# Kernel tuning notes

Measured on AMD Instinct MI355X. Metric: run time of the kernel, lower is better.

## Reference

```python
import jax, jax.numpy as jnp
import numpy as np

OUT_FEATURES = 8192
IN_FEATURES = 8192
BATCH = 512


def setup_inputs() -> dict:
    key = jax.random.key(0)
    k_x, k_w, k_s = jax.random.split(key, 3)
    x = jax.random.normal(k_x, (BATCH, IN_FEATURES), dtype=jnp.float32)
    # packed int4 weights: each int holds two nibbles (values 0..255)
    packed_weight = jax.random.randint(k_w, (OUT_FEATURES, IN_FEATURES // 2), 0, 256, dtype=jnp.int32)
    # per-output-row scale (positive, as produced by abs-max quantization)
    scale = jax.random.uniform(k_s, (OUT_FEATURES, 1), dtype=jnp.float32) * 0.02 + 1e-4
    return {"x": x, "packed_weight": packed_weight, "scale": scale}


def reference(x, packed_weight, scale):
    # Unpack two 4-bit values per byte: high nibble first (matches torch loop:
    # col i <- packed >> 4 & 15, col i+1 <- packed & 15), then subtract zero-point 8.
    hi = (packed_weight >> 4) & 15
    lo = packed_weight & 15
    q = jnp.stack([hi, lo], axis=-1).reshape(OUT_FEATURES, IN_FEATURES) - 8  # [out, in] int
    w = q.astype(scale.dtype) * scale  # dequantized weight [out, in]
    # linear: y = x @ W^T
    return jnp.einsum('bi,oi->bo', x, w)
```

## Files before the change

### kernel.cpp

```cpp
#include <hip/hip_runtime.h>
#include <cstdint>
#include <cstddef>

#define IN_F 8192
#define OUT_F 8192
#define BATCH 512
#define KSPLIT 2
#define KSLICE (IN_F / KSPLIT)
#define BK 64
#define TILES (KSLICE / BK)
#define BM 128
#define BN 256

typedef __bf16 bf16x8 __attribute__((ext_vector_type(8)));
typedef float floatx4 __attribute__((ext_vector_type(4)));

__device__ __forceinline__ ushort f2bf(float f) {
  uint32_t u = __float_as_uint(f);
  u += 0x7FFFu + ((u >> 16) & 1u);
  return (ushort)(u >> 16);
}

__device__ __forceinline__ uint32_t dq(int p) {
  uint32_t u = (uint32_t)p;
  return (((u >> 4) & 0xFu) | ((u & 0xFu) << 16)) | 0x43004300u;
}

__device__ __forceinline__ void gl16(const void* g, uint32_t* l) {
  __builtin_amdgcn_global_load_lds(
      (const __attribute__((address_space(1))) uint32_t*)g,
      (__attribute__((address_space(3))) uint32_t*)l, 16, 0, 0);
}

__global__ __launch_bounds__(256) void cvt_rowsum(const float* __restrict__ x,
                                                  ushort* __restrict__ xb,
                                                  float* __restrict__ rowsum,
                                                  float* __restrict__ zout) {
  const int b = blockIdx.x;
  const int t = threadIdx.x;
  const float4* xr = (const float4*)(x + (size_t)b * IN_F);
  ushort4* xo = (ushort4*)(xb + (size_t)b * IN_F);
  float s[2] = {0.f, 0.f};
#pragma unroll
  for (int i = 0; i < 8; ++i) {
    float4 v = xr[i * 256 + t];
    ushort4 o;
    o.x = f2bf(v.x); o.y = f2bf(v.y); o.z = f2bf(v.z); o.w = f2bf(v.w);
    xo[i * 256 + t] = o;
    if (zout) {
      float4 z = {0.f, 0.f, 0.f, 0.f};
      ((float4*)(zout + (size_t)b * OUT_F))[i * 256 + t] = z;
    }
    s[i >> 2] += __uint_as_float((uint32_t)o.x << 16) + __uint_as_float((uint32_t)o.y << 16)
               + __uint_as_float((uint32_t)o.z << 16) + __uint_as_float((uint32_t)o.w << 16);
  }
  __shared__ float red[4][2];
  const int lane = t & 63, wid = t >> 6;
#pragma unroll
  for (int j = 0; j < 2; ++j) {
    float v = s[j];
#pragma unroll
    for (int off = 32; off >= 1; off >>= 1) v += __shfl_down(v, off, 64);
    if (lane == 0) red[wid][j] = v;
  }
  __syncthreads();
  if (t < 2) rowsum[t * BATCH + b] = red[0][t] + red[1][t] + red[2][t] + red[3][t];
}

__global__ __launch_bounds__(512, 2) void qgemm(const ushort* __restrict__ xb,
                                                const int* __restrict__ pw,
                                                const float* __restrict__ scale,
                                                const float* __restrict__ rowsum,
                                                float* __restrict__ out,
                                                float* __restrict__ part) {
  __shared__ uint32_t As[2 * BM * 32];
  __shared__ uint32_t Bs[2 * BN * 32];

  const int tid = threadIdx.x;
  const int lane = tid & 63;
  const int w = tid >> 6;
  const int wm = w >> 2, wn = w & 3;
  const int lr = lane & 15, lq = lane >> 4;

  const int n0 = blockIdx.x * BN;
  const int m0 = blockIdx.y * BM;
  const int ks = blockIdx.z;

  const char* aSrc = (const char*)xb
      + (size_t)(m0 + w * 16 + (lane >> 3)) * (IN_F * 2)
      + (size_t)ks * (KSLICE * 2)
      + (size_t)((((lane & 7) ^ ((lane >> 3) & 7)) * 16));
  uint32_t* aDst = As + (w * 16) * 32;

  const int rt = tid >> 1;
  const int c0 = (tid & 1) * 2;
  const int rk = rt & 7;
  const int* bSrc = pw + (size_t)(n0 + rt) * (IN_F / 2) + ks * (KSLICE / 2);

  const int key = lr & 7;
  const int aOff = (wm * 64 + lr) * 32 + ((lq ^ key) * 4);
  const int bOff = (wn * 64 + lr) * 32 + ((lq ^ key) * 4);

  floatx4 acc[4][4] = {};

  auto stB = [&](int nb, int q, int4 p) {
    int4 u;
    u.x = dq(p.x); u.y = dq(p.y); u.z = dq(p.z); u.w = dq(p.w);
    *(int4*)(Bs + nb * 8192 + rt * 32 + ((q ^ rk) * 4)) = u;
  };

#define RD_BV(kh)                                                            \
  _Pragma("unroll") for (int fn = 0; fn < 4; ++fn)                           \
      bv[fn] = *(const bf16x8*)(Bs + (((bOff + fn * 512) ^ ((kh)*16)) + buf * 8192));
#define RD_AV(kh)                                                            \
  _Pragma("unroll") for (int fm = 0; fm < 4; ++fm)                           \
      av[fm] = *(const bf16x8*)(As + (((aOff + fm * 512) ^ ((kh)*16)) + buf * 4096));
#define MFMA_BLK()                                                           \
  __builtin_amdgcn_s_setprio(1);                                             \
  _Pragma("unroll") for (int fm = 0; fm < 4; ++fm)                           \
      _Pragma("unroll") for (int fn = 0; fn < 4; ++fn)                       \
          acc[fm][fn] = __builtin_amdgcn_mfma_f32_16x16x32_bf16(             \
              av[fm], bv[fn], acc[fm][fn], 0, 0, 0);                         \
  __builtin_amdgcn_s_setprio(0);

  {
    int4 p0 = *(const int4*)(bSrc + c0 * 4);
    int4 p1 = *(const int4*)(bSrc + c0 * 4 + 4);
    int4 p2 = *(const int4*)(bSrc + (c0 + 4) * 4);
    int4 p3 = *(const int4*)(bSrc + (c0 + 4) * 4 + 4);
    stB(0, c0, p0); stB(0, c0 + 1, p1); stB(0, c0 + 4, p2); stB(0, c0 + 5, p3);
    gl16(aSrc, aDst);
    gl16(aSrc + 131072, aDst + 256);
    asm volatile("s_waitcnt lgkmcnt(0)" ::: "memory");
  }

  for (int t = 0; t < TILES - 1; ++t) {
    const int buf = t & 1, nb = buf ^ 1;
    const int* bs = bSrc + (t + 1) * 32;
    int4 pb0 = *(const int4*)(bs + c0 * 4);
    int4 pb1 = *(const int4*)(bs + c0 * 4 + 4);
    int4 pb2 = *(const int4*)(bs + (c0 + 4) * 4);
    int4 pb3 = *(const int4*)(bs + (c0 + 4) * 4 + 4);
    const char* as = aSrc + (size_t)(t + 1) * 128;
    gl16(as, aDst + nb * 4096);
    gl16(as + 131072, aDst + nb * 4096 + 256);
    asm volatile("s_waitcnt vmcnt(6)" ::: "memory");
    asm volatile("s_barrier" ::: "memory");

    bf16x8 av[4], bv[4];
    RD_BV(0); RD_AV(0);
    MFMA_BLK();
    RD_BV(1); RD_AV(1);
    MFMA_BLK();
    stB(nb, c0, pb0); stB(nb, c0 + 1, pb1);
    stB(nb, c0 + 4, pb2); stB(nb, c0 + 5, pb3);

    asm volatile("s_waitcnt lgkmcnt(0)" ::: "memory");
    asm volatile("s_barrier" ::: "memory");
  }

  {
    const int buf = (TILES - 1) & 1;
    asm volatile("s_waitcnt vmcnt(0)" ::: "memory");
    asm volatile("s_barrier" ::: "memory");
    bf16x8 av[4], bv[4];
    RD_BV(0); RD_AV(0);
    MFMA_BLK();
    RD_BV(1); RD_AV(1);
    MFMA_BLK();
  }

  const int omb = m0 + wm * 64 + lq * 4;
  const int on = n0 + wn * 64 + lr;
  float scv[4];
#pragma unroll
  for (int fn = 0; fn < 4; ++fn) scv[fn] = scale[on + fn * 16];
  float rsv[4][4];
#pragma unroll
  for (int mi = 0; mi < 4; ++mi)
#pragma unroll
    for (int rr = 0; rr < 4; ++rr)
      rsv[mi][rr] = rowsum[ks * BATCH + omb + mi * 16 + rr];

  if (part) {
    float* dst = ks ? part : out;
#pragma unroll
    for (int mi = 0; mi < 4; ++mi)
#pragma unroll
      for (int fn = 0; fn < 4; ++fn) {
        const float s = scv[fn];
        float* op = dst + (size_t)(omb + mi * 16) * OUT_F + (on + fn * 16);
#pragma unroll
        for (int rr = 0; rr < 4; ++rr)
          op[(size_t)rr * OUT_F] = s * (acc[mi][fn][rr] - 136.f * rsv[mi][rr]);
      }
  } else {
#pragma unroll
    for (int mi = 0; mi < 4; ++mi)
#pragma unroll
      for (int fn = 0; fn < 4; ++fn) {
        const float s = scv[fn];
        float* op = out + (size_t)(omb + mi * 16) * OUT_F + (on + fn * 16);
#pragma unroll
        for (int rr = 0; rr < 4; ++rr)
          atomicAdd(op + (size_t)rr * OUT_F, s * (acc[mi][fn][rr] - 136.f * rsv[mi][rr]));
      }
  }
#undef RD_BV
#undef RD_AV
#undef MFMA_BLK
}

__global__ __launch_bounds__(256) void reduce_add(float* __restrict__ out,
                                                  const float* __restrict__ part) {
  const size_t n = (size_t)BATCH * OUT_F / 4;
  float4* o4 = (float4*)out;
  const float4* p4 = (const float4*)part;
  for (size_t i = (size_t)blockIdx.x * 256 + threadIdx.x; i < n;
       i += (size_t)gridDim.x * 256) {
    float4 a = o4[i];
    float4 b = p4[i];
    a.x += b.x; a.y += b.y; a.z += b.z; a.w += b.w;
    o4[i] = a;
  }
}

extern "C" void kernel_launch(void* const* d_in, const int* in_sizes, int n_in,
                              void* d_out, int out_size, void* d_ws, size_t ws_size,
                              hipStream_t stream) {
  const float* x = (const float*)d_in[0];
  const int* pw = (const int*)d_in[1];
  const float* scale = (const float*)d_in[2];
  float* out = (float*)d_out;

  ushort* xb = (ushort*)d_ws;
  float* rowsum = (float*)((char*)d_ws + (size_t)8 * 1024 * 1024);
  const size_t need = (size_t)8 * 1024 * 1024 + 65536 + (size_t)BATCH * OUT_F * 4;
  float* part = (ws_size >= need)
      ? (float*)((char*)d_ws + (size_t)8 * 1024 * 1024 + 65536)
      : nullptr;

  cvt_rowsum<<<BATCH, 256, 0, stream>>>(x, xb, rowsum, part ? nullptr : out);
  dim3 grid(OUT_F / BN, BATCH / BM, KSPLIT);
  qgemm<<<grid, 512, 0, stream>>>(xb, pw, scale, rowsum, out, part);
  if (part) reduce_add<<<2048, 256, 0, stream>>>(out, part);
}
```

Measured before the change: 304.8 us.

## Deepen qgemm pipeline with 4-stage A buffer and register-prefetched B tiles

Restructures the qgemm main loop into a deeper software pipeline. The A tile now has four LDS buffers loaded two tiles ahead via global_load_lds, and packed B weights are prefetched two tiles ahead into registers and dequantised into LDS one tile ahead. Extra barriers split each k-step into two MFMA phases, with the next tile's stores interleaved between them, to hide global-load latency behind MFMA work. This raises LDS use (extra 32KB for A) and register pressure, which could hurt occupancy at 2 blocks per CU, and the added barriers add synchronisation cost.

After: 304.9 us. No clear change (+0.1%).

```diff
diff --git a/kernel.cpp b/kernel.cpp
--- a/kernel.cpp
+++ b/kernel.cpp
@@ -73,7 +73,7 @@
                                                 const float* __restrict__ rowsum,
                                                 float* __restrict__ out,
                                                 float* __restrict__ part) {
-  __shared__ uint32_t As[2 * BM * 32];
+  __shared__ uint32_t As[4 * BM * 32];
   __shared__ uint32_t Bs[2 * BN * 32];
 
   const int tid = threadIdx.x;
@@ -103,71 +103,102 @@
 
   floatx4 acc[4][4] = {};
 
-  auto stB = [&](int nb, int q, int4 p) {
+  auto stB = [&](int bow, int q, int4 p) {
     int4 u;
     u.x = dq(p.x); u.y = dq(p.y); u.z = dq(p.z); u.w = dq(p.w);
-    *(int4*)(Bs + nb * 8192 + rt * 32 + ((q ^ rk) * 4)) = u;
+    *(int4*)(Bs + bow + rt * 32 + ((q ^ rk) * 4)) = u;
   };
 
-#define RD_BV(kh)                                                            \
-  _Pragma("unroll") for (int fn = 0; fn < 4; ++fn)                           \
-      bv[fn] = *(const bf16x8*)(Bs + (((bOff + fn * 512) ^ ((kh)*16)) + buf * 8192));
-#define RD_AV(kh)                                                            \
-  _Pragma("unroll") for (int fm = 0; fm < 4; ++fm)                           \
-      av[fm] = *(const bf16x8*)(As + (((aOff + fm * 512) ^ ((kh)*16)) + buf * 4096));
-#define MFMA_BLK()                                                           \
+#define DSREAD(kh, AO, BO)                                                   \
+  _Pragma("unroll") for (int f = 0; f < 4; ++f)                              \
+      av[f] = *(const bf16x8*)(As + (((aOff + f * 512) ^ ((kh)*16)) + (AO))); \
+  _Pragma("unroll") for (int f = 0; f < 4; ++f)                              \
+      bv[f] = *(const bf16x8*)(Bs + (((bOff + f * 512) ^ ((kh)*16)) + (BO)));
+#define MFMA16()                                                             \
   __builtin_amdgcn_s_setprio(1);                                             \
   _Pragma("unroll") for (int fm = 0; fm < 4; ++fm)                           \
       _Pragma("unroll") for (int fn = 0; fn < 4; ++fn)                       \
           acc[fm][fn] = __builtin_amdgcn_mfma_f32_16x16x32_bf16(             \
               av[fm], bv[fn], acc[fm][fn], 0, 0, 0);                         \
   __builtin_amdgcn_s_setprio(0);
+#define BAR() asm volatile("s_barrier" ::: "memory")
+#define LGKM0()                                                              \
+  asm volatile("s_waitcnt lgkmcnt(0)" ::: "memory");                         \
+  __builtin_amdgcn_sched_barrier(0)
+
+  int4 pbC0, pbC1, pbC2, pbC3, pbN0, pbN1, pbN2, pbN3;
 
   {
-    int4 p0 = *(const int4*)(bSrc + c0 * 4);
-    int4 p1 = *(const int4*)(bSrc + c0 * 4 + 4);
-    int4 p2 = *(const int4*)(bSrc + (c0 + 4) * 4);
-    int4 p3 = *(const int4*)(bSrc + (c0 + 4) * 4 + 4);
-    stB(0, c0, p0); stB(0, c0 + 1, p1); stB(0, c0 + 4, p2); stB(0, c0 + 5, p3);
     gl16(aSrc, aDst);
     gl16(aSrc + 131072, aDst + 256);
-    asm volatile("s_waitcnt lgkmcnt(0)" ::: "memory");
-  }
-
-  for (int t = 0; t < TILES - 1; ++t) {
-    const int buf = t & 1, nb = buf ^ 1;
-    const int* bs = bSrc + (t + 1) * 32;
-    int4 pb0 = *(const int4*)(bs + c0 * 4);
-    int4 pb1 = *(const int4*)(bs + c0 * 4 + 4);
-    int4 pb2 = *(const int4*)(bs + (c0 + 4) * 4);
-    int4 pb3 = *(const int4*)(bs + (c0 + 4) * 4 + 4);
-    const char* as = aSrc + (size_t)(t + 1) * 128;
-    gl16(as, aDst + nb * 4096);
-    gl16(as + 131072, aDst + nb * 4096 + 256);
+    gl16(aSrc + 128, aDst + 4096);
+    gl16(aSrc + 128 + 131072, aDst + 4096 + 256);
+    int4 q0 = *(const int4*)(bSrc + c0 * 4);
+    int4 q1 = *(const int4*)(bSrc + c0 * 4 + 4);
+    int4 q2 = *(const int4*)(bSrc + (c0 + 4) * 4);
+    int4 q3 = *(const int4*)(bSrc + (c0 + 4) * 4 + 4);
+    stB(0, c0, q0); stB(0, c0 + 1, q1); stB(0, c0 + 4, q2); stB(0, c0 + 5, q3);
+    const int* b1 = bSrc + 32;
+    pbC0 = *(const int4*)(b1 + c0 * 4);
+    pbC1 = *(const int4*)(b1 + c0 * 4 + 4);
+    pbC2 = *(const int4*)(b1 + (c0 + 4) * 4);
+    pbC3 = *(const int4*)(b1 + (c0 + 4) * 4 + 4);
+    asm volatile("s_waitcnt vmcnt(0) lgkmcnt(0)" ::: "memory");
+    BAR();
+  }
+
+  for (int t = 0; t <= TILES - 3; ++t) {
+    const int AO = (t & 3) * 4096, BO = (t & 1) * 8192;
+    const int AOs = ((t + 2) & 3) * 4096, BOw = ((t + 1) & 1) * 8192;
+    bf16x8 av[4], bv[4];
+    const int* bs = bSrc + (t + 2) * 32;
+    pbN0 = *(const int4*)(bs + c0 * 4);
+    pbN1 = *(const int4*)(bs + c0 * 4 + 4);
+    pbN2 = *(const int4*)(bs + (c0 + 4) * 4);
+    pbN3 = *(const int4*)(bs + (c0 + 4) * 4 + 4);
+    DSREAD(0, AO, BO);
+    BAR(); LGKM0();
+    MFMA16();
+    BAR();
+    const char* as = aSrc + (size_t)(t + 2) * 128;
+    gl16(as, aDst + AOs);
+    gl16(as + 131072, aDst + AOs + 256);
+    stB(BOw, c0, pbC0); stB(BOw, c0 + 1, pbC1);
+    stB(BOw, c0 + 4, pbC2); stB(BOw, c0 + 5, pbC3);
+    DSREAD(1, AO, BO);
+    BAR(); LGKM0();
+    MFMA16();
     asm volatile("s_waitcnt vmcnt(6)" ::: "memory");
-    asm volatile("s_barrier" ::: "memory");
-
+    BAR();
+    pbC0 = pbN0; pbC1 = pbN1; pbC2 = pbN2; pbC3 = pbN3;
+  }
+
+  {
+    const int AO = ((TILES - 2) & 3) * 4096, BO = ((TILES - 2) & 1) * 8192;
+    const int BOw = ((TILES - 1) & 1) * 8192;
     bf16x8 av[4], bv[4];
-    RD_BV(0); RD_AV(0);
-    MFMA_BLK();
-    RD_BV(1); RD_AV(1);
-    MFMA_BLK();
-    stB(nb, c0, pb0); stB(nb, c0 + 1, pb1);
-    stB(nb, c0 + 4, pb2); stB(nb, c0 + 5, pb3);
-
-    asm volatile("s_waitcnt lgkmcnt(0)" ::: "memory");
-    asm volatile("s_barrier" ::: "memory");
-  }
-
+    DSREAD(0, AO, BO);
+    BAR(); LGKM0();
+    MFMA16();
+    BAR();
+    stB(BOw, c0, pbC0); stB(BOw, c0 + 1, pbC1);
+    stB(BOw, c0 + 4, pbC2); stB(BOw, c0 + 5, pbC3);
+    DSREAD(1, AO, BO);
+    BAR(); LGKM0();
+    MFMA16();
+    asm volatile("s_waitcnt vmcnt(0)" ::: "memory");
+    BAR();
+  }
   {
-    const int buf = (TILES - 1) & 1;
-    asm volatile("s_waitcnt vmcnt(0)" ::: "memory");
-    asm volatile("s_barrier" ::: "memory");
+    const int AO = ((TILES - 1) & 3) * 4096, BO = ((TILES - 1) & 1) * 8192;
     bf16x8 av[4], bv[4];
-    RD_BV(0); RD_AV(0);
-    MFMA_BLK();
-    RD_BV(1); RD_AV(1);
-    MFMA_BLK();
+    DSREAD(0, AO, BO);
+    BAR(); LGKM0();
+    MFMA16();
+    BAR();
+    DSREAD(1, AO, BO);
+    LGKM0();
+    MFMA16();
   }
 
   const int omb = m0 + wm * 64 + lq * 4;
@@ -206,9 +237,10 @@
           atomicAdd(op + (size_t)rr * OUT_F, s * (acc[mi][fn][rr] - 136.f * rsv[mi][rr]));
       }
   }
-#undef RD_BV
-#undef RD_AV
-#undef MFMA_BLK
+#undef DSREAD
+#undef MFMA16
+#undef BAR
+#undef LGKM0
 }
 
 __global__ __launch_bounds__(256) void reduce_add(float* __restrict__ out,
```

## Load packed weights directly into LDS with 4-stage async pipeline and dequant in registers

Applied to the files above, without the earlier changes.

The GEMM kernel is restructured to bring both activations and packed int4 weights into LDS with async global_load_lds through a 4-slot ring buffer. Weights are dequantized to bf16 in registers after the LDS read, using a cheaper nibble-extraction expression, instead of being dequantized before the LDS store. The tile grows to 256x256 with BK 32 and the K-split rises to 4, so rowsum and the reduction kernel are extended to handle three partial buffers. The aim is to hide global-load latency and remove the synchronous weight load-then-store stage, at the cost of more accumulator registers, a larger workspace and more partial-sum traffic.

Result: faster. 284.9 us (-6.5%).

```diff
diff --git a/kernel.cpp b/kernel.cpp
--- a/kernel.cpp
+++ b/kernel.cpp
@@ -5,11 +5,11 @@
 #define IN_F 8192
 #define OUT_F 8192
 #define BATCH 512
-#define KSPLIT 2
+#define KSPLIT 4
 #define KSLICE (IN_F / KSPLIT)
-#define BK 64
+#define BK 32
 #define TILES (KSLICE / BK)
-#define BM 128
+#define BM 256
 #define BN 256
 
 typedef __bf16 bf16x8 __attribute__((ext_vector_type(8)));
@@ -21,9 +21,8 @@
   return (ushort)(u >> 16);
 }
 
-__device__ __forceinline__ uint32_t dq(int p) {
-  uint32_t u = (uint32_t)p;
-  return (((u >> 4) & 0xFu) | ((u & 0xFu) << 16)) | 0x43004300u;
+__device__ __forceinline__ uint32_t dq(uint32_t u) {
+  return (((u | (u << 20)) >> 4) & 0x000F000Fu) | 0x43004300u;
 }
 
 __device__ __forceinline__ void gl16(const void* g, uint32_t* l) {
@@ -40,7 +39,7 @@
   const int t = threadIdx.x;
   const float4* xr = (const float4*)(x + (size_t)b * IN_F);
   ushort4* xo = (ushort4*)(xb + (size_t)b * IN_F);
-  float s[2] = {0.f, 0.f};
+  float s[4] = {0.f, 0.f, 0.f, 0.f};
 #pragma unroll
   for (int i = 0; i < 8; ++i) {
     float4 v = xr[i * 256 + t];
@@ -51,20 +50,20 @@
       float4 z = {0.f, 0.f, 0.f, 0.f};
       ((float4*)(zout + (size_t)b * OUT_F))[i * 256 + t] = z;
     }
-    s[i >> 2] += __uint_as_float((uint32_t)o.x << 16) + __uint_as_float((uint32_t)o.y << 16)
+    s[i >> 1] += __uint_as_float((uint32_t)o.x << 16) + __uint_as_float((uint32_t)o.y << 16)
                + __uint_as_float((uint32_t)o.z << 16) + __uint_as_float((uint32_t)o.w << 16);
   }
-  __shared__ float red[4][2];
+  __shared__ float red[4][4];
   const int lane = t & 63, wid = t >> 6;
 #pragma unroll
-  for (int j = 0; j < 2; ++j) {
+  for (int j = 0; j < 4; ++j) {
     float v = s[j];
 #pragma unroll
     for (int off = 32; off >= 1; off >>= 1) v += __shfl_down(v, off, 64);
     if (lane == 0) red[wid][j] = v;
   }
   __syncthreads();
-  if (t < 2) rowsum[t * BATCH + b] = red[0][t] + red[1][t] + red[2][t] + red[3][t];
+  if (t < 4) rowsum[t * BATCH + b] = red[0][t] + red[1][t] + red[2][t] + red[3][t];
 }
 
 __global__ __launch_bounds__(512, 2) void qgemm(const ushort* __restrict__ xb,
@@ -73,8 +72,8 @@
                                                 const float* __restrict__ rowsum,
                                                 float* __restrict__ out,
                                                 float* __restrict__ part) {
-  __shared__ uint32_t As[2 * BM * 32];
-  __shared__ uint32_t Bs[2 * BN * 32];
+  __shared__ uint32_t As[4 * 256 * 16];
+  __shared__ uint32_t Bs[4 * 256 * 16];
 
   const int tid = threadIdx.x;
   const int lane = tid & 63;
@@ -86,141 +85,214 @@
   const int m0 = blockIdx.y * BM;
   const int ks = blockIdx.z;
 
-  const char* aSrc = (const char*)xb
-      + (size_t)(m0 + w * 16 + (lane >> 3)) * (IN_F * 2)
-      + (size_t)ks * (KSLICE * 2)
-      + (size_t)((((lane & 7) ^ ((lane >> 3) & 7)) * 16));
-  uint32_t* aDst = As + (w * 16) * 32;
-
-  const int rt = tid >> 1;
-  const int c0 = (tid & 1) * 2;
-  const int rk = rt & 7;
-  const int* bSrc = pw + (size_t)(n0 + rt) * (IN_F / 2) + ks * (KSLICE / 2);
-
-  const int key = lr & 7;
-  const int aOff = (wm * 64 + lr) * 32 + ((lq ^ key) * 4);
-  const int bOff = (wn * 64 + lr) * 32 + ((lq ^ key) * 4);
-
-  floatx4 acc[4][4] = {};
-
-  auto stB = [&](int nb, int q, int4 p) {
-    int4 u;
-    u.x = dq(p.x); u.y = dq(p.y); u.z = dq(p.z); u.w = dq(p.w);
-    *(int4*)(Bs + nb * 8192 + rt * 32 + ((q ^ rk) * 4)) = u;
-  };
-
-#define RD_BV(kh)                                                            \
-  _Pragma("unroll") for (int fn = 0; fn < 4; ++fn)                           \
-      bv[fn] = *(const bf16x8*)(Bs + (((bOff + fn * 512) ^ ((kh)*16)) + buf * 8192));
-#define RD_AV(kh)                                                            \
-  _Pragma("unroll") for (int fm = 0; fm < 4; ++fm)                           \
-      av[fm] = *(const bf16x8*)(As + (((aOff + fm * 512) ^ ((kh)*16)) + buf * 4096));
-#define MFMA_BLK()                                                           \
-  __builtin_amdgcn_s_setprio(1);                                             \
-  _Pragma("unroll") for (int fm = 0; fm < 4; ++fm)                           \
-      _Pragma("unroll") for (int fn = 0; fn < 4; ++fn)                       \
-          acc[fm][fn] = __builtin_amdgcn_mfma_f32_16x16x32_bf16(             \
-              av[fm], bv[fn], acc[fm][fn], 0, 0, 0);                         \
-  __builtin_amdgcn_s_setprio(0);
+  const int swz = ((lane & 3) ^ ((lane >> 3) & 3)) * 16;
+  const char* aSrc0 = (const char*)xb
+      + (size_t)(m0 + w * 32 + (lane >> 2)) * (IN_F * 2)
+      + (size_t)ks * (KSLICE * 2) + swz;
+  const char* bSrc0 = (const char*)pw
+      + (size_t)(n0 + w * 32 + (lane >> 2)) * (IN_F * 2)
+      + (size_t)ks * (KSLICE * 2) + swz;
+  uint32_t* aD = As + w * 512;
+  uint32_t* bD = Bs + w * 512;
+
+  const int key = (lr >> 1) & 3;
+  const int aBase = wm * 2048 + lr * 16 + ((lq ^ key) * 4);
+  const int bBase = wn * 1024 + lr * 16 + ((lq ^ key) * 4);
+
+  floatx4 acc[8][4] = {};
+
+#define BAR() asm volatile("s_barrier" ::: "memory")
+#define LGKM0()                                                              \
+  asm volatile("s_waitcnt lgkmcnt(0)" ::: "memory");                         \
+  __builtin_amdgcn_sched_barrier(0)
+#define VMW(n) asm volatile("s_waitcnt vmcnt(" #n ")" ::: "memory")
+
+  gl16(aSrc0, aD);              gl16(aSrc0 + 262144, aD + 256);
+  gl16(bSrc0, bD);              gl16(bSrc0 + 262144, bD + 256);
+  gl16(aSrc0 + 64, aD + 4096);  gl16(aSrc0 + 64 + 262144, aD + 4096 + 256);
+  gl16(bSrc0 + 64, bD + 4096);  gl16(bSrc0 + 64 + 262144, bD + 4096 + 256);
+  VMW(4);
+  BAR();
+
+  bf16x8 av[4], bv[4];
+  int4 pb[4];
+
+  for (int t = 0; t <= TILES - 3; ++t) {
+    const int slot = (t & 3) * 4096, wsl = ((t + 2) & 3) * 4096;
+    const char* as = aSrc0 + (size_t)(t + 2) * 64;
+    const char* bs = bSrc0 + (size_t)(t + 2) * 64;
+#pragma unroll
+    for (int f = 0; f < 4; ++f)
+      pb[f] = *(const int4*)(Bs + slot + bBase + f * 256);
+#pragma unroll
+    for (int f = 0; f < 4; ++f)
+      av[f] = *(const bf16x8*)(As + slot + aBase + f * 256);
+    gl16(as, aD + wsl);
+    gl16(as + 262144, aD + wsl + 256);
+    BAR();
+    LGKM0();
+#pragma unroll
+    for (int f = 0; f < 4; ++f) {
+      int4 u;
+      u.x = (int)dq((uint32_t)pb[f].x); u.y = (int)dq((uint32_t)pb[f].y);
+      u.z = (int)dq((uint32_t)pb[f].z); u.w = (int)dq((uint32_t)pb[f].w);
+      bv[f] = *(const bf16x8*)&u;
+    }
+    __builtin_amdgcn_s_setprio(1);
+#pragma unroll
+    for (int fm = 0; fm < 4; ++fm)
+#pragma unroll
+      for (int fn = 0; fn < 4; ++fn)
+        acc[fm][fn] = __builtin_amdgcn_mfma_f32_16x16x32_bf16(av[fm], bv[fn],
+                                                              acc[fm][fn], 0, 0, 0);
+    __builtin_amdgcn_s_setprio(0);
+    BAR();
+#pragma unroll
+    for (int f = 0; f < 4; ++f)
+      av[f] = *(const bf16x8*)(As + slot + aBase + 1024 + f * 256);
+    gl16(bs, bD + wsl);
+    gl16(bs + 262144, bD + wsl + 256);
+    BAR();
+    LGKM0();
+    __builtin_amdgcn_s_setprio(1);
+#pragma unroll
+    for (int fm = 0; fm < 4; ++fm)
+#pragma unroll
+      for (int fn = 0; fn < 4; ++fn)
+        acc[4 + fm][fn] = __builtin_amdgcn_mfma_f32_16x16x32_bf16(av[fm], bv[fn],
+                                                                  acc[4 + fm][fn], 0, 0, 0);
+    __builtin_amdgcn_s_setprio(0);
+    VMW(4);
+    BAR();
+  }
 
   {
-    int4 p0 = *(const int4*)(bSrc + c0 * 4);
-    int4 p1 = *(const int4*)(bSrc + c0 * 4 + 4);
-    int4 p2 = *(const int4*)(bSrc + (c0 + 4) * 4);
-    int4 p3 = *(const int4*)(bSrc + (c0 + 4) * 4 + 4);
-    stB(0, c0, p0); stB(0, c0 + 1, p1); stB(0, c0 + 4, p2); stB(0, c0 + 5, p3);
-    gl16(aSrc, aDst);
-    gl16(aSrc + 131072, aDst + 256);
-    asm volatile("s_waitcnt lgkmcnt(0)" ::: "memory");
-  }
-
-  for (int t = 0; t < TILES - 1; ++t) {
-    const int buf = t & 1, nb = buf ^ 1;
-    const int* bs = bSrc + (t + 1) * 32;
-    int4 pb0 = *(const int4*)(bs + c0 * 4);
-    int4 pb1 = *(const int4*)(bs + c0 * 4 + 4);
-    int4 pb2 = *(const int4*)(bs + (c0 + 4) * 4);
-    int4 pb3 = *(const int4*)(bs + (c0 + 4) * 4 + 4);
-    const char* as = aSrc + (size_t)(t + 1) * 128;
-    gl16(as, aDst + nb * 4096);
-    gl16(as + 131072, aDst + nb * 4096 + 256);
-    asm volatile("s_waitcnt vmcnt(6)" ::: "memory");
-    asm volatile("s_barrier" ::: "memory");
-
-    bf16x8 av[4], bv[4];
-    RD_BV(0); RD_AV(0);
-    MFMA_BLK();
-    RD_BV(1); RD_AV(1);
-    MFMA_BLK();
-    stB(nb, c0, pb0); stB(nb, c0 + 1, pb1);
-    stB(nb, c0 + 4, pb2); stB(nb, c0 + 5, pb3);
-
-    asm volatile("s_waitcnt lgkmcnt(0)" ::: "memory");
-    asm volatile("s_barrier" ::: "memory");
-  }
-
+    const int slot = ((TILES - 2) & 3) * 4096;
+#pragma unroll
+    for (int f = 0; f < 4; ++f)
+      pb[f] = *(const int4*)(Bs + slot + bBase + f * 256);
+#pragma unroll
+    for (int f = 0; f < 4; ++f)
+      av[f] = *(const bf16x8*)(As + slot + aBase + f * 256);
+    BAR();
+    LGKM0();
+#pragma unroll
+    for (int f = 0; f < 4; ++f) {
+      int4 u;
+      u.x = (int)dq((uint32_t)pb[f].x); u.y = (int)dq((uint32_t)pb[f].y);
+      u.z = (int)dq((uint32_t)pb[f].z); u.w = (int)dq((uint32_t)pb[f].w);
+      bv[f] = *(const bf16x8*)&u;
+    }
+#pragma unroll
+    for (int fm = 0; fm < 4; ++fm)
+#pragma unroll
+      for (int fn = 0; fn < 4; ++fn)
+        acc[fm][fn] = __builtin_amdgcn_mfma_f32_16x16x32_bf16(av[fm], bv[fn],
+                                                              acc[fm][fn], 0, 0, 0);
+    BAR();
+#pragma unroll
+    for (int f = 0; f < 4; ++f)
+      av[f] = *(const bf16x8*)(As + slot + aBase + 1024 + f * 256);
+    LGKM0();
+#pragma unroll
+    for (int fm = 0; fm < 4; ++fm)
+#pragma unroll
+      for (int fn = 0; fn < 4; ++fn)
+        acc[4 + fm][fn] = __builtin_amdgcn_mfma_f32_16x16x32_bf16(av[fm], bv[fn],
+                                                                  acc[4 + fm][fn], 0, 0, 0);
+    VMW(0);
+    BAR();
+  }
   {
-    const int buf = (TILES - 1) & 1;
-    asm volatile("s_waitcnt vmcnt(0)" ::: "memory");
-    asm volatile("s_barrier" ::: "memory");
-    bf16x8 av[4], bv[4];
-    RD_BV(0); RD_AV(0);
-    MFMA_BLK();
-    RD_BV(1); RD_AV(1);
-    MFMA_BLK();
-  }
-
-  const int omb = m0 + wm * 64 + lq * 4;
+    const int slot = ((TILES - 1) & 3) * 4096;
+#pragma unroll
+    for (int f = 0; f < 4; ++f)
+      pb[f] = *(const int4*)(Bs + slot + bBase + f * 256);
+#pragma unroll
+    for (int f = 0; f < 4; ++f)
+      av[f] = *(const bf16x8*)(As + slot + aBase + f * 256);
+    LGKM0();
+#pragma unroll
+    for (int f = 0; f < 4; ++f) {
+      int4 u;
+      u.x = (int)dq((uint32_t)pb[f].x); u.y = (int)dq((uint32_t)pb[f].y);
+      u.z = (int)dq((uint32_t)pb[f].z); u.w = (int)dq((uint32_t)pb[f].w);
+      bv[f] = *(const bf16x8*)&u;
+    }
+#pragma unroll
+    for (int fm = 0; fm < 4; ++fm)
+#pragma unroll
+      for (int fn = 0; fn < 4; ++fn)
+        acc[fm][fn] = __builtin_amdgcn_mfma_f32_16x16x32_bf16(av[fm], bv[fn],
+                                                              acc[fm][fn], 0, 0, 0);
+#pragma unroll
+    for (int f = 0; f < 4; ++f)
+      av[f] = *(const bf16x8*)(As + slot + aBase + 1024 + f * 256);
+    LGKM0();
+#pragma unroll
+    for (int fm = 0; fm < 4; ++fm)
+#pragma unroll
+      for (int fn = 0; fn < 4; ++fn)
+        acc[4 + fm][fn] = __builtin_amdgcn_mfma_f32_16x16x32_bf16(av[fm], bv[fn],
+                                                                  acc[4 + fm][fn], 0, 0, 0);
+  }
+
+  const int omb = m0 + wm * 128 + lq * 4;
   const int on = n0 + wn * 64 + lr;
   float scv[4];
 #pragma unroll
   for (int fn = 0; fn < 4; ++fn) scv[fn] = scale[on + fn * 16];
-  float rsv[4][4];
-#pragma unroll
-  for (int mi = 0; mi < 4; ++mi)
+  float rsv[8][4];
+#pragma unroll
+  for (int fmg = 0; fmg < 8; ++fmg)
 #pragma unroll
     for (int rr = 0; rr < 4; ++rr)
-      rsv[mi][rr] = rowsum[ks * BATCH + omb + mi * 16 + rr];
+      rsv[fmg][rr] = rowsum[ks * BATCH + omb + fmg * 16 + rr];
 
   if (part) {
-    float* dst = ks ? part : out;
-#pragma unroll
-    for (int mi = 0; mi < 4; ++mi)
+    float* dst = (ks == 0) ? out : (part + (size_t)(ks - 1) * BATCH * OUT_F);
+#pragma unroll
+    for (int fmg = 0; fmg < 8; ++fmg)
 #pragma unroll
       for (int fn = 0; fn < 4; ++fn) {
         const float s = scv[fn];
-        float* op = dst + (size_t)(omb + mi * 16) * OUT_F + (on + fn * 16);
+        float* op = dst + (size_t)(omb + fmg * 16) * OUT_F + (on + fn * 16);
 #pragma unroll
         for (int rr = 0; rr < 4; ++rr)
-          op[(size_t)rr * OUT_F] = s * (acc[mi][fn][rr] - 136.f * rsv[mi][rr]);
+          op[(size_t)rr * OUT_F] = s * (acc[fmg][fn][rr] - 136.f * rsv[fmg][rr]);
       }
   } else {
 #pragma unroll
-    for (int mi = 0; mi < 4; ++mi)
+    for (int fmg = 0; fmg < 8; ++fmg)
 #pragma unroll
       for (int fn = 0; fn < 4; ++fn) {
         const float s = scv[fn];
-        float* op = out + (size_t)(omb + mi * 16) * OUT_F + (on + fn * 16);
+        float* op = out + (size_t)(omb + fmg * 16) * OUT_F + (on + fn * 16);
 #pragma unroll
         for (int rr = 0; rr < 4; ++rr)
-          atomicAdd(op + (size_t)rr * OUT_F, s * (acc[mi][fn][rr] - 136.f * rsv[mi][rr]));
+          atomicAdd(op + (size_t)rr * OUT_F, s * (acc[fmg][fn][rr] - 136.f * rsv[fmg][rr]));
       }
   }
-#undef RD_BV
-#undef RD_AV
-#undef MFMA_BLK
+#undef BAR
+#undef LGKM0
+#undef VMW
 }
 
 __global__ __launch_bounds__(256) void reduce_add(float* __restrict__ out,
                                                   const float* __restrict__ part) {
   const size_t n = (size_t)BATCH * OUT_F / 4;
   float4* o4 = (float4*)out;
-  const float4* p4 = (const float4*)part;
+  const float4* p0 = (const float4*)part;
+  const float4* p1 = p0 + n;
+  const float4* p2 = p1 + n;
   for (size_t i = (size_t)blockIdx.x * 256 + threadIdx.x; i < n;
        i += (size_t)gridDim.x * 256) {
     float4 a = o4[i];
-    float4 b = p4[i];
-    a.x += b.x; a.y += b.y; a.z += b.z; a.w += b.w;
+    float4 b = p0[i], c = p1[i], d = p2[i];
+    a.x += b.x + c.x + d.x;
+    a.y += b.y + c.y + d.y;
+    a.z += b.z + c.z + d.z;
+    a.w += b.w + c.w + d.w;
     o4[i] = a;
   }
 }
@@ -235,7 +307,8 @@
 
   ushort* xb = (ushort*)d_ws;
   float* rowsum = (float*)((char*)d_ws + (size_t)8 * 1024 * 1024);
-  const size_t need = (size_t)8 * 1024 * 1024 + 65536 + (size_t)BATCH * OUT_F * 4;
+  const size_t need = (size_t)8 * 1024 * 1024 + 65536
+      + (size_t)3 * BATCH * OUT_F * sizeof(float);
   float* part = (ws_size >= need)
       ? (float*)((char*)d_ws + (size_t)8 * 1024 * 1024 + 65536)
       : nullptr;
```
